# Kernel optimization log

Measured on AMD Instinct MI355X. Metric: run time of the kernel, lower is better.

Reference implementation:

```python
import jax, jax.numpy as jnp
import numpy as np

N, E, H, CIN = 10000, 320000, 4, 64
NT, ET = 8, 22
C1 = CIN          # per-head dim layer1 -> concat gives H*C1 = 256
C2 = H * CIN      # per-head dim layer2 = 256, mean over heads -> 256


def _hgat_layer(x, edge_index, node_type, edge_attr, edge_type,
                W, b, Wedge, ntemb, etemb, asrc, adst, aedge, res_proj, concat):
    Nn = x.shape[0]
    Hh, Cc = asrc.shape
    src, dst = edge_index[0], edge_index[1]
    # node-type conditioned transform: [N, H, C]
    xh = ((x + ntemb[node_type]) @ W).reshape(Nn, Hh, Cc)
    # edge features with edge-type embedding: [E, H, C]
    e = (edge_attr @ Wedge + etemb[edge_type]).reshape(-1, Hh, Cc)
    xs = xh[src]                     # [E, H, C] gather
    xd = xh[dst]                     # [E, H, C] gather
    logits = jax.nn.leaky_relu(
        (xs * asrc).sum(-1) + (xd * adst).sum(-1) + (e * aedge).sum(-1),
        negative_slope=0.2)          # [E, H]
    # segment softmax over incoming edges of each dst node
    m = jax.ops.segment_max(logits, dst, num_segments=Nn)   # [N, H]
    m = jnp.where(jnp.isfinite(m), m, jnp.zeros_like(m))
    p = jnp.exp(logits - m[dst])                            # [E, H]
    denom = jax.ops.segment_sum(p, dst, num_segments=Nn)    # [N, H]
    alpha = p / (denom[dst] + 1e-16)                        # [E, H]
    msg = alpha[..., None] * (xs + e)                       # [E, H, C]
    out = jax.ops.segment_sum(msg, dst, num_segments=Nn)    # [N, H, C]
    out = out.reshape(Nn, Hh * Cc) if concat else out.mean(axis=1)
    out = out + b
    res = x @ res_proj if res_proj is not None else x
    return out + res


def setup_inputs() -> dict:
    key = jax.random.key(0)
    ks = jax.random.split(key, 24)

    def rn(k, shape, fan_in):
        return jax.random.normal(k, shape, jnp.float32) * (fan_in ** -0.5)

    x = jax.random.normal(ks[0], (N, CIN), jnp.float32)
    edge_index = jax.random.randint(ks[1], (2, E), 0, N, jnp.int64)
    node_type = jax.random.randint(ks[2], (N,), 0, NT, jnp.int64)
    edge_attr = jax.random.normal(ks[3], (E, CIN), jnp.float32)
    edge_type = jax.random.randint(ks[4], (E,), 0, ET, jnp.int64)

    inp = dict(x=x, edge_index=edge_index, node_type=node_type,
               edge_attr=edge_attr, edge_type=edge_type)
    # layer 1: in=CIN, per-head C1, concat -> H*C1
    inp.update(
        l1_W=rn(ks[5], (CIN, H * C1), CIN),
        l1_b=rn(ks[6], (H * C1,), H * C1),
        l1_Wedge=rn(ks[7], (CIN, H * C1), CIN),
        l1_ntemb=rn(ks[8], (NT, CIN), CIN),
        l1_etemb=rn(ks[9], (ET, H * C1), H * C1),
        l1_asrc=rn(ks[10], (H, C1), C1),
        l1_adst=rn(ks[11], (H, C1), C1),
        l1_aedge=rn(ks[12], (H, C1), C1),
        l1_res=rn(ks[13], (CIN, H * C1), CIN),
    )
    # layer 2: in=H*C1, per-head C2, mean over heads -> C2
    inp.update(
        l2_W=rn(ks[14], (H * C1, H * C2), H * C1),
        l2_b=rn(ks[15], (C2,), C2),
        l2_Wedge=rn(ks[16], (CIN, H * C2), CIN),
        l2_ntemb=rn(ks[17], (NT, H * C1), H * C1),
        l2_etemb=rn(ks[18], (ET, H * C2), H * C2),
        l2_asrc=rn(ks[19], (H, C2), C2),
        l2_adst=rn(ks[20], (H, C2), C2),
        l2_aedge=rn(ks[21], (H, C2), C2),
    )
    return inp


def reference(x, edge_index, node_type, edge_attr, edge_type,
              l1_W, l1_b, l1_Wedge, l1_ntemb, l1_etemb, l1_asrc, l1_adst, l1_aedge, l1_res,
              l2_W, l2_b, l2_Wedge, l2_ntemb, l2_etemb, l2_asrc, l2_adst, l2_aedge):
    h = _hgat_layer(x, edge_index, node_type, edge_attr, edge_type,
                    l1_W, l1_b, l1_Wedge, l1_ntemb, l1_etemb,
                    l1_asrc, l1_adst, l1_aedge, l1_res, concat=True)
    h = jax.nn.relu(h)
    out = _hgat_layer(h, edge_index, node_type, edge_attr, edge_type,
                      l2_W, l2_b, l2_Wedge, l2_ntemb, l2_etemb,
                      l2_asrc, l2_adst, l2_aedge, None, concat=False)
    return out
```

## Files before the change

### kernel.cpp

```cpp
#include <hip/hip_runtime.h>
#include <stdint.h>

#define NN   10000
#define NE   320000
#define K1   704
#define K2V  1408

typedef unsigned short u16;
typedef unsigned int   u32;

__device__ __forceinline__ float b2f(u16 v){ u32 u = ((u32)v) << 16; return __uint_as_float(u); }
__device__ __forceinline__ u16 f2b(float f){
  u32 u = __float_as_uint(f);
  u32 r = (u + 0x7fffu + ((u >> 16) & 1u)) >> 16;
  return (u16)r;
}
__device__ __forceinline__ float ldf(const void* p, size_t i, int bf){
  if (bf){ u32 u = ((u32)((const u16*)p)[i]) << 16; return __uint_as_float(u); }
  return ((const float*)p)[i];
}
__device__ __forceinline__ int geti(const int* p, size_t i, int w64){
  return w64 ? p[2 * i] : p[i];
}

#define FW_W1A  0
#define FW_W1D  256
#define FW_WA12 512
#define FW_ETA1 1024
#define FW_ETA2 1112
#define FW_NTS1 1200
#define FW_NTD1 1232
#define FW_W2A  1264
#define FW_W2D  2288
#define FW_NTS2 3312
#define FW_NTD2 3344

#define WS_FLG   0u
#define WS_DEG   16u
#define WS_OFF   40016u
#define WS_CUR   80032u
#define WS_META  120032u
#define WS_EL    5240032u
#define WS_S1    15480032u
#define WS_D1    15640032u
#define WS_S2    15800032u
#define WS_D2    15960032u
#define WS_FW    16120032u
#define WS_M1T   16136032u
#define WS_M2T   16496480u
#define WS_HBUF  17217376u
#define WS_V     22337376u

__global__ void k_probe(const u16* x16, const int* ei, const int* nt, const int* et, int4* flg){
  if (threadIdx.x == 0 && blockIdx.x == 0){
    int okb = 1;
    for (int i = 0; i < 64; i++){
      u16 u = x16[i]; int e = (u >> 7) & 0xFF;
      if (!(e >= 90 && e <= 160)){ okb = 0; break; }
    }
    int ei64 = 1, nt64 = 1, et64 = 1;
    for (int i = 0; i < 32; i++){
      if (ei[2 * i + 1] != 0) ei64 = 0;
      if (nt[2 * i + 1] != 0) nt64 = 0;
      if (et[2 * i + 1] != 0) et64 = 0;
    }
    int4 f; f.x = okb; f.y = ei64; f.z = nt64; f.w = et64;
    *flg = f;
  }
}

__global__ void k_zero(int* deg){
  int t = blockIdx.x * 256 + threadIdx.x;
  if (t < NN) deg[t] = 0;
}

__global__ void k_hist(const int* ei, int* deg, const int4* flg){
  int4 f = *flg;
  int e = blockIdx.x * 256 + threadIdx.x;
  if (e < NE){ int dst = geti(ei, NE + e, f.y); atomicAdd(&deg[dst], 1); }
}

__global__ void k_scan(const int* deg, int* off, int* cursor){
  __shared__ int part[256];
  int t = threadIdx.x;
  int base = t * 40;
  int s = 0;
  for (int i = 0; i < 40; i++){ int idx = base + i; s += (idx < NN) ? deg[idx] : 0; }
  part[t] = s;
  __syncthreads();
  for (int d = 1; d < 256; d <<= 1){
    int v = (t >= d) ? part[t - d] : 0;
    __syncthreads();
    part[t] += v;
    __syncthreads();
  }
  int run = (t == 0) ? 0 : part[t - 1];
  for (int i = 0; i < 40; i++){
    int idx = base + i;
    if (idx < NN){ off[idx] = run; cursor[idx] = run; run += deg[idx]; }
  }
  if (t == 255) off[NN] = part[255];
}

__global__ void k_scatter(const int* ei, const int* ntype, const int* etype,
                          int* cursor, int4* meta, const int4* flg){
  int4 f = *flg;
  int e = blockIdx.x * 256 + threadIdx.x;
  if (e < NE){
    int src = geti(ei, e, f.y), dst = geti(ei, NE + e, f.y);
    int pos = atomicAdd(&cursor[dst], 1);
    int4 m; m.x = e; m.y = src; m.z = geti(etype, e, f.w); m.w = geti(ntype, src, f.z);
    meta[pos] = m;
  }
}

__global__ void k_fold_a(const void* W1, const void* Wedge1, const void* asrc1, const void* adst1,
                         const void* aedge1, const void* etemb1,
                         const void* W2, const void* Wedge2, const void* asrc2, const void* adst2,
                         const void* aedge2, const void* etemb2, float* fw, const int4* flg){
  int bf = flg->x;
  int s = blockIdx.x * 256 + threadIdx.x;
  if (s < 256){
    int k = s >> 2, h = s & 3; float a = 0.f, d = 0.f;
    for (int c = 0; c < 64; c++){
      float w = ldf(W1, k * 256 + h * 64 + c, bf);
      a += w * ldf(asrc1, h * 64 + c, bf); d += w * ldf(adst1, h * 64 + c, bf);
    }
    fw[FW_W1A + k * 4 + h] = a; fw[FW_W1D + k * 4 + h] = d;
  } else if (s < 768){
    int q = s - 256; int k = q >> 3, dd = q & 7; float a = 0.f;
    if (dd < 4){
      for (int c = 0; c < 64; c++) a += ldf(Wedge1, k * 256 + dd * 64 + c, bf) * ldf(aedge1, dd * 64 + c, bf);
    } else {
      int h = dd - 4;
      for (int c = 0; c < 256; c++) a += ldf(Wedge2, k * 1024 + h * 256 + c, bf) * ldf(aedge2, h * 256 + c, bf);
    }
    fw[FW_WA12 + k * 8 + dd] = a;
  } else if (s < 856){
    int q = s - 768; int te = q >> 2, h = q & 3; float a = 0.f;
    for (int c = 0; c < 64; c++) a += ldf(etemb1, te * 256 + h * 64 + c, bf) * ldf(aedge1, h * 64 + c, bf);
    fw[FW_ETA1 + te * 4 + h] = a;
  } else if (s < 944){
    int q = s - 856; int te = q >> 2, h = q & 3; float a = 0.f;
    for (int c = 0; c < 256; c++) a += ldf(etemb2, te * 1024 + h * 256 + c, bf) * ldf(aedge2, h * 256 + c, bf);
    fw[FW_ETA2 + te * 4 + h] = a;
  } else if (s < 1968){
    int q = s - 944; int k = q >> 2, h = q & 3; float a = 0.f, d = 0.f;
    for (int c = 0; c < 256; c++){
      float w = ldf(W2, k * 1024 + h * 256 + c, bf);
      a += w * ldf(asrc2, h * 256 + c, bf); d += w * ldf(adst2, h * 256 + c, bf);
    }
    fw[FW_W2A + k * 4 + h] = a; fw[FW_W2D + k * 4 + h] = d;
  }
}

__global__ void k_fold_b(const void* ntemb1, const void* ntemb2, float* fw, const int4* flg){
  int bf = flg->x;
  int t = threadIdx.x;
  if (t < 32){
    int te = t >> 2, h = t & 3; float a = 0.f, d = 0.f;
    for (int k = 0; k < 64; k++){
      float x = ldf(ntemb1, te * 64 + k, bf);
      a += x * fw[FW_W1A + k * 4 + h]; d += x * fw[FW_W1D + k * 4 + h];
    }
    fw[FW_NTS1 + te * 4 + h] = a; fw[FW_NTD1 + te * 4 + h] = d;
  } else {
    int q = t - 32; int te = q >> 2, h = q & 3; float a = 0.f, d = 0.f;
    for (int k = 0; k < 256; k++){
      float x = ldf(ntemb2, te * 256 + k, bf);
      a += x * fw[FW_W2A + k * 4 + h]; d += x * fw[FW_W2D + k * 4 + h];
    }
    fw[FW_NTS2 + te * 4 + h] = a; fw[FW_NTD2 + te * 4 + h] = d;
  }
}

__global__ void k_m1t(const void* W1, const void* Wedge1, const void* ntemb1, const void* etemb1,
                      const void* res1, const void* b1, u16* M1T, const int4* flg){
  int bf = flg->x;
  int c = blockIdx.x; int t = threadIdx.x; int ch = c >> 6;
  for (int r = t; r < K1; r += 256){
    float v = 0.f;
    if (r < 256){ int h = r >> 6, k = r & 63; v = (h == ch) ? ldf(W1, k * 256 + c, bf) : 0.f; }
    else if (r < 512){ int q = r - 256; int h = q >> 6, k = q & 63; v = (h == ch) ? ldf(Wedge1, k * 256 + c, bf) : 0.f; }
    else if (r < 544){ int q = r - 512; int h = q >> 3, te = q & 7;
      if (h == ch){ float a = 0.f; for (int k = 0; k < 64; k++) a += ldf(ntemb1, te * 64 + k, bf) * ldf(W1, k * 256 + c, bf); v = a; } }
    else if (r < 632){ int q = r - 544; int h = q / 22, te = q % 22; v = (h == ch) ? ldf(etemb1, te * 256 + c, bf) : 0.f; }
    else if (r < 696){ int k = r - 632; v = ldf(res1, k * 256 + c, bf); }
    else if (r == 696){ v = ldf(b1, c, bf); }
    M1T[c * K1 + r] = f2b(v);
  }
}

__global__ void k_m2t(const void* W2, const void* Wedge2, const void* ntemb2, const void* etemb2,
                      const void* b2, u16* M2T, const int4* flg){
  int bf = flg->x;
  int c = blockIdx.x; int t = threadIdx.x;
  for (int r = t; r < K2V; r += 256){
    float v = 0.f;
    if (r < 1024){ int h = r >> 8, k = r & 255; v = 0.25f * ldf(W2, k * 1024 + h * 256 + c, bf); }
    else if (r < 1280){ int q = r - 1024; int h = q >> 6, k = q & 63; v = 0.25f * ldf(Wedge2, k * 1024 + h * 256 + c, bf); }
    else if (r < 1312){ int q = r - 1280; int h = q >> 3, te = q & 7; float a = 0.f;
      for (int k = 0; k < 256; k++) a += ldf(ntemb2, te * 256 + k, bf) * ldf(W2, k * 1024 + h * 256 + c, bf);
      v = 0.25f * a; }
    else if (r < 1400){ int q = r - 1312; int h = q / 22, te = q % 22; v = 0.25f * ldf(etemb2, te * 1024 + h * 256 + c, bf); }
    else if (r == 1400){ v = ldf(b2, c, bf); }
    M2T[c * K2V + r] = f2b(v);
  }
}

__global__ void k_sd1(const void* x, const int* ntype, const float* fw, float* s1, float* d1,
                      const int4* flg){
  int4 f = *flg;
  int id = blockIdx.x * 256 + threadIdx.x;
  if (id >= NN * 4) return;
  int n = id >> 2, h = id & 3;
  float a = 0.f, d = 0.f;
  for (int k = 0; k < 64; k++){
    float xv = ldf(x, (size_t)n * 64 + k, f.x);
    a += xv * fw[FW_W1A + k * 4 + h]; d += xv * fw[FW_W1D + k * 4 + h];
  }
  int nt = geti(ntype, n, f.z);
  s1[id] = a + fw[FW_NTS1 + nt * 4 + h];
  d1[id] = d + fw[FW_NTD1 + nt * 4 + h];
}

__global__ void k_sd2(const u16* hbuf, const int* ntype, const float* fw, float* s2, float* d2,
                      const int4* flg){
  int4 f = *flg;
  int id = blockIdx.x * 256 + threadIdx.x;
  if (id >= NN * 4) return;
  int n = id >> 2, h = id & 3;
  float a = 0.f, d = 0.f;
  for (int k = 0; k < 256; k++){
    float xv = b2f(hbuf[n * 256 + k]);
    a += xv * fw[FW_W2A + k * 4 + h]; d += xv * fw[FW_W2D + k * 4 + h];
  }
  int nt = geti(ntype, n, f.z);
  s2[id] = a + fw[FW_NTS2 + nt * 4 + h];
  d2[id] = d + fw[FW_NTD2 + nt * 4 + h];
}

__global__ void k_el(const void* ea, const int* etype, const float* fw, float* el, const int4* flg){
  __shared__ float sw[512];
  __shared__ float sea[32 * 65];
  int4 f = *flg;
  int t = threadIdx.x;
  for (int i = t; i < 512; i += 256) sw[i] = fw[FW_WA12 + i];
  int e0 = blockIdx.x * 32;
  {
    int eloc = t >> 3, kc = (t & 7) * 8;
    float* dp = &sea[eloc * 65 + kc];
    if (f.x){
      const u16* p = (const u16*)ea + (size_t)(e0 + eloc) * 64 + kc;
      ushort4 a = *(const ushort4*)p;
      ushort4 b = *(const ushort4*)(p + 4);
      dp[0] = b2f(a.x); dp[1] = b2f(a.y); dp[2] = b2f(a.z); dp[3] = b2f(a.w);
      dp[4] = b2f(b.x); dp[5] = b2f(b.y); dp[6] = b2f(b.z); dp[7] = b2f(b.w);
    } else {
      const float* p = (const float*)ea + (size_t)(e0 + eloc) * 64 + kc;
      float4 a = *(const float4*)p;
      float4 b = *(const float4*)(p + 4);
      dp[0] = a.x; dp[1] = a.y; dp[2] = a.z; dp[3] = a.w;
      dp[4] = b.x; dp[5] = b.y; dp[6] = b.z; dp[7] = b.w;
    }
  }
  __syncthreads();
  int eloc = t >> 3, d = t & 7;
  int e = e0 + eloc;
  float a = 0.f;
  for (int k = 0; k < 64; k++) a += sea[eloc * 65 + k] * sw[k * 8 + d];
  int et = geti(etype, e, f.w);
  a += (d < 4) ? fw[FW_ETA1 + et * 4 + d] : fw[FW_ETA2 + et * 4 + (d - 4)];
  el[(size_t)e * 8 + d] = a;
}

__global__ __launch_bounds__(256) void k_agg1(const int* off, const int4* meta,
    const float* el, const float* s1, const float* d1,
    const void* x, const void* ea, u16* V1, const int4* flg){
  int bf = flg->x;
  int n = blockIdx.x * 4 + (threadIdx.x >> 6);
  int lane = threadIdx.x & 63;
  int beg = off[n], end = off[n + 1];
  float4 dv = *(const float4*)&d1[n * 4];
  float dvh[4] = {dv.x, dv.y, dv.z, dv.w};

  int ht1 = lane >> 3;
  int c1  = lane & 7;
  int ht2a = lane / 22;
  int c2a  = lane - 22 * ht2a;
  bool v2b = (lane >= 2 && lane < 24);
  int c2b  = lane - 2;

  float den[4] = {0.f, 0.f, 0.f, 0.f};
  float g1[4] = {0.f, 0.f, 0.f, 0.f};
  float g2[4] = {0.f, 0.f, 0.f, 0.f};
  float t1 = 0.f, t2a = 0.f, t2b = 0.f;
#pragma unroll 2
  for (int i = beg; i < end; i++){
    int4 md = meta[i];
    int eid = md.x, src = md.y, et = md.z, nt = md.w;
    float4 elv = *(const float4*)&el[(size_t)eid * 8];
    float4 sv  = *(const float4*)&s1[src * 4];
    float lg[4] = {sv.x + dvh[0] + elv.x, sv.y + dvh[1] + elv.y,
                   sv.z + dvh[2] + elv.z, sv.w + dvh[3] + elv.w};
    float pa[4];
#pragma unroll
    for (int h = 0; h < 4; h++){
      float l = lg[h]; l = fmaxf(l, 0.2f * l);
      float p = __expf(l);
      den[h] += p; pa[h] = p;
    }
    float xv = ldf(x, (size_t)src * 64 + lane, bf);
    float ev = ldf(ea, (size_t)eid * 64 + lane, bf);
#pragma unroll
    for (int h = 0; h < 4; h++){ g1[h] += pa[h] * xv; g2[h] += pa[h] * ev; }
    float pt1 = (ht1 & 2) ? ((ht1 & 1) ? pa[3] : pa[2]) : ((ht1 & 1) ? pa[1] : pa[0]);
    t1  += ((ht1 < 4) && (nt == c1)) ? pt1 : 0.f;
    float p2a = (ht2a == 2) ? pa[2] : ((ht2a == 1) ? pa[1] : pa[0]);
    t2a += (et == c2a) ? p2a : 0.f;
    t2b += (v2b && (et == c2b)) ? pa[3] : 0.f;
  }
  float inv[4];
#pragma unroll
  for (int h = 0; h < 4; h++)
    inv[h] = (den[h] > 0.f) ? 1.f / (den[h] + 1e-16f) : 0.f;

  u16* vrow = &V1[(size_t)n * K1];
#pragma unroll
  for (int h = 0; h < 4; h++){
    vrow[h * 64 + lane]       = f2b(inv[h] * g1[h]);
    vrow[256 + h * 64 + lane] = f2b(inv[h] * g2[h]);
  }
  if (lane < 32) vrow[512 + lane] = f2b(inv[lane >> 3] * t1);
  vrow[544 + lane] = f2b(inv[ht2a] * t2a);
  if (lane < 24) vrow[608 + lane] = f2b(inv[3] * t2b * ((lane >= 2) ? 1.f : 0.f) + ((lane < 2) ? inv[2] * t2b : 0.f));
  vrow[632 + lane] = f2b(ldf(x, (size_t)n * 64 + lane, bf));
  if (lane == 0) vrow[696] = f2b(1.f);
  if (lane >= 1 && lane < 8) vrow[696 + lane] = 0;
}

__global__ __launch_bounds__(256) void k_agg2(const int* off, const int4* meta,
    const float* el, const float* s2, const float* d2,
    const u16* hbuf, const void* ea, u16* V2, int nbase, const int4* flg){
  int bf = flg->x;
  int nl = blockIdx.x * 4 + (threadIdx.x >> 6);
  int n = nbase + nl;
  int lane = threadIdx.x & 63;
  int beg = off[n], end = off[n + 1];
  float4 dv = *(const float4*)&d2[n * 4];
  float dvh[4] = {dv.x, dv.y, dv.z, dv.w};

  int ht1 = lane >> 3;
  int c1  = lane & 7;
  int ht2a = lane / 22;
  int c2a  = lane - 22 * ht2a;
  bool v2b = (lane >= 2 && lane < 24);
  int c2b  = lane - 2;

  float den[4] = {0.f, 0.f, 0.f, 0.f};
  float g3[4][4] = {};
  float g4[4] = {0.f, 0.f, 0.f, 0.f};
  float t3 = 0.f, t4a = 0.f, t4b = 0.f;
#pragma unroll 2
  for (int i = beg; i < end; i++){
    int4 md = meta[i];
    int eid = md.x, src = md.y, et = md.z, nt = md.w;
    float4 elv = *(const float4*)&el[(size_t)eid * 8 + 4];
    float4 sv  = *(const float4*)&s2[src * 4];
    float lg[4] = {sv.x + dvh[0] + elv.x, sv.y + dvh[1] + elv.y,
                   sv.z + dvh[2] + elv.z, sv.w + dvh[3] + elv.w};
    float pa[4];
#pragma unroll
    for (int h = 0; h < 4; h++){
      float l = lg[h]; l = fmaxf(l, 0.2f * l);
      float p = __expf(l);
      den[h] += p; pa[h] = p;
    }
    ushort4 hv = *(const ushort4*)&hbuf[(size_t)src * 256 + lane * 4];
    float h0 = b2f(hv.x), h1 = b2f(hv.y), h2 = b2f(hv.z), h3 = b2f(hv.w);
    float ev = ldf(ea, (size_t)eid * 64 + lane, bf);
#pragma unroll
    for (int h = 0; h < 4; h++){
      float p = pa[h];
      g3[h][0] += p * h0; g3[h][1] += p * h1; g3[h][2] += p * h2; g3[h][3] += p * h3;
      g4[h] += p * ev;
    }
    float pt1 = (ht1 & 2) ? ((ht1 & 1) ? pa[3] : pa[2]) : ((ht1 & 1) ? pa[1] : pa[0]);
    t3  += ((ht1 < 4) && (nt == c1)) ? pt1 : 0.f;
    float p2a = (ht2a == 2) ? pa[2] : ((ht2a == 1) ? pa[1] : pa[0]);
    t4a += (et == c2a) ? p2a : 0.f;
    t4b += (v2b && (et == c2b)) ? pa[3] : 0.f;
  }
  float inv[4];
#pragma unroll
  for (int h = 0; h < 4; h++)
    inv[h] = (den[h] > 0.f) ? 1.f / (den[h] + 1e-16f) : 0.f;

  u16* vrow = &V2[(size_t)nl * K2V];
#pragma unroll
  for (int h = 0; h < 4; h++){
#pragma unroll
    for (int j = 0; j < 4; j++)
      vrow[h * 256 + lane * 4 + j] = f2b(inv[h] * g3[h][j]);
    vrow[1024 + h * 64 + lane] = f2b(inv[h] * g4[h]);
  }
  if (lane < 32) vrow[1280 + lane] = f2b(inv[lane >> 3] * t3);
  vrow[1312 + lane] = f2b(inv[ht2a] * t4a);
  if (lane < 24) vrow[1376 + lane] = f2b(inv[3] * t4b * ((lane >= 2) ? 1.f : 0.f) + ((lane < 2) ? inv[2] * t4b : 0.f));
  if (lane == 0) vrow[1400] = f2b(1.f);
  if (lane >= 1 && lane < 8) vrow[1400 + lane] = 0;
}

typedef __bf16 bf16x8 __attribute__((ext_vector_type(8)));
typedef float  f32x4  __attribute__((ext_vector_type(4)));

template<int KK, int MODE>
__global__ __launch_bounds__(256) void k_gemm(const u16* A, const u16* Bt,
                                              const u16* hres, void* outv,
                                              int rowbase, int mcount){
  __shared__ __align__(16) u16 As[64 * 40];
  __shared__ __align__(16) u16 Bs[64 * 40];
  int t = threadIdx.x;
  int w = t >> 6, lane = t & 63;
  int m0 = blockIdx.x * 64, n0 = blockIdx.y * 64;
  int wm = w & 1, wn = w >> 1;
  f32x4 acc[2][2] = {};
  int ar = t >> 2, akc = (t & 3) * 8;
  for (int k0 = 0; k0 < KK; k0 += 32){
    {
      int row = m0 + ar;
      ushort4 v0 = {0, 0, 0, 0}, v1 = {0, 0, 0, 0};
      if (row < mcount){
        const u16* p = &A[(size_t)row * KK + k0 + akc];
        v0 = *(const ushort4*)p; v1 = *(const ushort4*)(p + 4);
      }
      *(ushort4*)&As[ar * 40 + akc] = v0;
      *(ushort4*)&As[ar * 40 + akc + 4] = v1;
      const u16* q = &Bt[(size_t)(n0 + ar) * KK + k0 + akc];
      ushort4 b0 = *(const ushort4*)q;
      ushort4 b1 = *(const ushort4*)(q + 4);
      *(ushort4*)&Bs[ar * 40 + akc] = b0;
      *(ushort4*)&Bs[ar * 40 + akc + 4] = b1;
    }
    __syncthreads();
    int kq = (lane >> 4) * 8;
    int ml = lane & 15;
    bf16x8 a0 = *(const bf16x8*)&As[(wm * 32 + ml) * 40 + kq];
    bf16x8 a1 = *(const bf16x8*)&As[(wm * 32 + 16 + ml) * 40 + kq];
    bf16x8 b0 = *(const bf16x8*)&Bs[(wn * 32 + ml) * 40 + kq];
    bf16x8 b1 = *(const bf16x8*)&Bs[(wn * 32 + 16 + ml) * 40 + kq];
    acc[0][0] = __builtin_amdgcn_mfma_f32_16x16x32_bf16(a0, b0, acc[0][0], 0, 0, 0);
    acc[0][1] = __builtin_amdgcn_mfma_f32_16x16x32_bf16(a0, b1, acc[0][1], 0, 0, 0);
    acc[1][0] = __builtin_amdgcn_mfma_f32_16x16x32_bf16(a1, b0, acc[1][0], 0, 0, 0);
    acc[1][1] = __builtin_amdgcn_mfma_f32_16x16x32_bf16(a1, b1, acc[1][1], 0, 0, 0);
    __syncthreads();
  }
  int quad = lane >> 4, col4 = lane & 15;
#pragma unroll
  for (int i = 0; i < 2; i++)
#pragma unroll
    for (int j = 0; j < 2; j++){
      int colG = n0 + wn * 32 + j * 16 + col4;
#pragma unroll
      for (int r = 0; r < 4; r++){
        int rowL = m0 + wm * 32 + i * 16 + quad * 4 + r;
        if (rowL < mcount){
          int rowG = rowbase + rowL;
          float v = acc[i][j][r];
          if (MODE == 1){
            v = fmaxf(v, 0.f);
            ((u16*)outv)[(size_t)rowG * 256 + colG] = f2b(v);
          } else {
            v += b2f(hres[(size_t)rowG * 256 + colG]);
            ((float*)outv)[(size_t)rowG * 256 + colG] = v;
          }
        }
      }
    }
}

extern "C" void kernel_launch(void* const* d_in, const int* in_sizes, int n_in,
                              void* d_out, int out_size, void* d_ws, size_t ws_size,
                              hipStream_t stream){
  const void* x      = d_in[0];
  const int*  ei     = (const int*)d_in[1];
  const int*  ntype  = (const int*)d_in[2];
  const void* ea     = d_in[3];
  const int*  etype  = (const int*)d_in[4];
  const void* l1_W     = d_in[5];
  const void* l1_b     = d_in[6];
  const void* l1_Wedge = d_in[7];
  const void* l1_ntemb = d_in[8];
  const void* l1_etemb = d_in[9];
  const void* l1_asrc  = d_in[10];
  const void* l1_adst  = d_in[11];
  const void* l1_aedge = d_in[12];
  const void* l1_res   = d_in[13];
  const void* l2_W     = d_in[14];
  const void* l2_b     = d_in[15];
  const void* l2_Wedge = d_in[16];
  const void* l2_ntemb = d_in[17];
  const void* l2_etemb = d_in[18];
  const void* l2_asrc  = d_in[19];
  const void* l2_adst  = d_in[20];
  const void* l2_aedge = d_in[21];

  char* ws = (char*)d_ws;
  int4*  flg    = (int4*)(ws + WS_FLG);
  int*   deg    = (int*)(ws + WS_DEG);
  int*   off    = (int*)(ws + WS_OFF);
  int*   cur    = (int*)(ws + WS_CUR);
  int4*  meta   = (int4*)(ws + WS_META);
  float* el     = (float*)(ws + WS_EL);
  float* s1     = (float*)(ws + WS_S1);
  float* d1     = (float*)(ws + WS_D1);
  float* s2     = (float*)(ws + WS_S2);
  float* d2     = (float*)(ws + WS_D2);
  float* fw     = (float*)(ws + WS_FW);
  u16*   M1T    = (u16*)(ws + WS_M1T);
  u16*   M2T    = (u16*)(ws + WS_M2T);
  u16*   hbuf   = (u16*)(ws + WS_HBUF);
  u16*   V      = (u16*)(ws + WS_V);

  hipLaunchKernelGGL(k_probe,   dim3(1),    dim3(64),  0, stream,
                     (const u16*)x, ei, ntype, etype, flg);
  hipLaunchKernelGGL(k_zero,    dim3(40),   dim3(256), 0, stream, deg);
  hipLaunchKernelGGL(k_hist,    dim3(1250), dim3(256), 0, stream, ei, deg, flg);
  hipLaunchKernelGGL(k_scan,    dim3(1),    dim3(256), 0, stream, deg, off, cur);
  hipLaunchKernelGGL(k_scatter, dim3(1250), dim3(256), 0, stream, ei, ntype, etype, cur, meta, flg);
  hipLaunchKernelGGL(k_fold_a,  dim3(8),    dim3(256), 0, stream,
                     l1_W, l1_Wedge, l1_asrc, l1_adst, l1_aedge, l1_etemb,
                     l2_W, l2_Wedge, l2_asrc, l2_adst, l2_aedge, l2_etemb, fw, flg);
  hipLaunchKernelGGL(k_fold_b,  dim3(1),    dim3(64),  0, stream, l1_ntemb, l2_ntemb, fw, flg);
  hipLaunchKernelGGL(k_m1t,     dim3(256),  dim3(256), 0, stream,
                     l1_W, l1_Wedge, l1_ntemb, l1_etemb, l1_res, l1_b, M1T, flg);
  hipLaunchKernelGGL(k_m2t,     dim3(256),  dim3(256), 0, stream,
                     l2_W, l2_Wedge, l2_ntemb, l2_etemb, l2_b, M2T, flg);
  hipLaunchKernelGGL(k_sd1,     dim3(157),  dim3(256), 0, stream, x, ntype, fw, s1, d1, flg);
  hipLaunchKernelGGL(k_el,      dim3(10000),dim3(256), 0, stream, ea, etype, fw, el, flg);
  hipLaunchKernelGGL(k_agg1,    dim3(2500), dim3(256), 0, stream, off, meta, el, s1, d1, x, ea, V, flg);
  hipLaunchKernelGGL((k_gemm<K1, 1>),  dim3(157, 4), dim3(256), 0, stream, V, M1T, hbuf, (void*)hbuf, 0, NN);
  hipLaunchKernelGGL(k_sd2,     dim3(157),  dim3(256), 0, stream, hbuf, ntype, fw, s2, d2, flg);
  for (int c = 0; c < 2; c++){
    int base = c * 5000;
    hipLaunchKernelGGL(k_agg2,  dim3(1250), dim3(256), 0, stream,
                       off, meta, el, s2, d2, hbuf, ea, V, base, flg);
    hipLaunchKernelGGL((k_gemm<K2V, 2>), dim3(79, 4), dim3(256), 0, stream,
                       V, M2T, hbuf, d_out, base, 5000);
  }
}
```

Baseline: 606.0 us.

## Precompute per-edge attention exponentials in edge order and cache bf16 edge features

```diff
diff --git a/kernel.cpp b/kernel.cpp
--- a/kernel.cpp
+++ b/kernel.cpp
@@ -40,7 +40,8 @@
 #define WS_OFF   40016u
 #define WS_CUR   80032u
 #define WS_META  120032u
-#define WS_EL    5240032u
+#define WS_P1    5240032u
+#define WS_EL2   10360032u
 #define WS_S1    15480032u
 #define WS_D1    15640032u
 #define WS_S2    15800032u
@@ -50,6 +51,8 @@
 #define WS_M2T   16496480u
 #define WS_HBUF  17217376u
 #define WS_V     22337376u
+#define WS_EA16  36417376u
+#define WS_NEED16 77377376ull
 
 __global__ void k_probe(const u16* x16, const int* ei, const int* nt, const int* et, int4* flg){
   if (threadIdx.x == 0 && blockIdx.x == 0){
@@ -240,7 +243,9 @@
   d2[id] = d + fw[FW_NTD2 + nt * 4 + h];
 }
 
-__global__ void k_el(const void* ea, const int* etype, const float* fw, float* el, const int4* flg){
+__global__ void k_el(const void* ea, const int* etype, const int* ei,
+                     const float* s1, const float* d1, const float* fw,
+                     float* p1, float* el2, u16* ea16, const int4* flg){
   __shared__ float sw[512];
   __shared__ float sea[32 * 65];
   int4 f = *flg;
@@ -249,19 +254,30 @@
   int e0 = blockIdx.x * 32;
   {
     int eloc = t >> 3, kc = (t & 7) * 8;
-    float* dp = &sea[eloc * 65 + kc];
+    int e = e0 + eloc;
+    float v[8];
     if (f.x){
-      const u16* p = (const u16*)ea + (size_t)(e0 + eloc) * 64 + kc;
+      const u16* p = (const u16*)ea + (size_t)e * 64 + kc;
       ushort4 a = *(const ushort4*)p;
       ushort4 b = *(const ushort4*)(p + 4);
-      dp[0] = b2f(a.x); dp[1] = b2f(a.y); dp[2] = b2f(a.z); dp[3] = b2f(a.w);
-      dp[4] = b2f(b.x); dp[5] = b2f(b.y); dp[6] = b2f(b.z); dp[7] = b2f(b.w);
+      v[0] = b2f(a.x); v[1] = b2f(a.y); v[2] = b2f(a.z); v[3] = b2f(a.w);
+      v[4] = b2f(b.x); v[5] = b2f(b.y); v[6] = b2f(b.z); v[7] = b2f(b.w);
     } else {
-      const float* p = (const float*)ea + (size_t)(e0 + eloc) * 64 + kc;
+      const float* p = (const float*)ea + (size_t)e * 64 + kc;
       float4 a = *(const float4*)p;
       float4 b = *(const float4*)(p + 4);
-      dp[0] = a.x; dp[1] = a.y; dp[2] = a.z; dp[3] = a.w;
-      dp[4] = b.x; dp[5] = b.y; dp[6] = b.z; dp[7] = b.w;
+      v[0] = a.x; v[1] = a.y; v[2] = a.z; v[3] = a.w;
+      v[4] = b.x; v[5] = b.y; v[6] = b.z; v[7] = b.w;
+    }
+    float* dp = &sea[eloc * 65 + kc];
+#pragma unroll
+    for (int j = 0; j < 8; j++) dp[j] = v[j];
+    if (ea16){
+      ushort4 o0, o1;
+      o0.x = f2b(v[0]); o0.y = f2b(v[1]); o0.z = f2b(v[2]); o0.w = f2b(v[3]);
+      o1.x = f2b(v[4]); o1.y = f2b(v[5]); o1.z = f2b(v[6]); o1.w = f2b(v[7]);
+      *(ushort4*)&ea16[(size_t)e * 64 + kc]     = o0;
+      *(ushort4*)&ea16[(size_t)e * 64 + kc + 4] = o1;
     }
   }
   __syncthreads();
@@ -270,26 +286,45 @@
   float a = 0.f;
   for (int k = 0; k < 64; k++) a += sea[eloc * 65 + k] * sw[k * 8 + d];
   int et = geti(etype, e, f.w);
-  a += (d < 4) ? fw[FW_ETA1 + et * 4 + d] : fw[FW_ETA2 + et * 4 + (d - 4)];
-  el[(size_t)e * 8 + d] = a;
+  if (d < 4){
+    a += fw[FW_ETA1 + et * 4 + d];
+    int src = geti(ei, e, f.y), dst = geti(ei, NE + e, f.y);
+    float l = s1[src * 4 + d] + d1[dst * 4 + d] + a;
+    l = fmaxf(l, 0.2f * l);
+    p1[(size_t)e * 4 + d] = __expf(l);
+  } else {
+    a += fw[FW_ETA2 + et * 4 + (d - 4)];
+    el2[(size_t)e * 4 + (d - 4)] = a;
+  }
+}
+
+__global__ void k_p2(const int* ei, const float* el2, const float* s2, const float* d2,
+                     float* p2, const int4* flg){
+  int4 f = *flg;
+  int idx = blockIdx.x * 256 + threadIdx.x;
+  if (idx >= NE * 4) return;
+  int e = idx >> 2, h = idx & 3;
+  int src = geti(ei, e, f.y), dst = geti(ei, NE + e, f.y);
+  float l = s2[src * 4 + h] + d2[dst * 4 + h] + el2[idx];
+  l = fmaxf(l, 0.2f * l);
+  p2[idx] = __expf(l);
 }
 
 __global__ __launch_bounds__(256) void k_agg1(const int* off, const int4* meta,
-    const float* el, const float* s1, const float* d1,
-    const void* x, const void* ea, u16* V1, const int4* flg){
+    const float* p1, const void* x, const void* ea, const u16* ea16,
+    u16* V1, const int4* flg){
   int bf = flg->x;
   int n = blockIdx.x * 4 + (threadIdx.x >> 6);
   int lane = threadIdx.x & 63;
   int beg = off[n], end = off[n + 1];
-  float4 dv = *(const float4*)&d1[n * 4];
-  float dvh[4] = {dv.x, dv.y, dv.z, dv.w};
 
   int ht1 = lane >> 3;
   int c1  = lane & 7;
   int ht2a = lane / 22;
   int c2a  = lane - 22 * ht2a;
-  bool v2b = (lane >= 2 && lane < 24);
-  int c2b  = lane - 2;
+  int hb   = (lane < 2) ? 2 : 3;
+  int cb   = (lane < 2) ? (20 + lane) : (lane - 2);
+  bool vb  = (lane < 24);
 
   float den[4] = {0.f, 0.f, 0.f, 0.f};
   float g1[4] = {0.f, 0.f, 0.f, 0.f};
@@ -299,26 +334,19 @@
   for (int i = beg; i < end; i++){
     int4 md = meta[i];
     int eid = md.x, src = md.y, et = md.z, nt = md.w;
-    float4 elv = *(const float4*)&el[(size_t)eid * 8];
-    float4 sv  = *(const float4*)&s1[src * 4];
-    float lg[4] = {sv.x + dvh[0] + elv.x, sv.y + dvh[1] + elv.y,
-                   sv.z + dvh[2] + elv.z, sv.w + dvh[3] + elv.w};
-    float pa[4];
-#pragma unroll
-    for (int h = 0; h < 4; h++){
-      float l = lg[h]; l = fmaxf(l, 0.2f * l);
-      float p = __expf(l);
-      den[h] += p; pa[h] = p;
-    }
+    float4 p4 = *(const float4*)&p1[(size_t)eid * 4];
+    float pa[4] = {p4.x, p4.y, p4.z, p4.w};
+    den[0] += pa[0]; den[1] += pa[1]; den[2] += pa[2]; den[3] += pa[3];
     float xv = ldf(x, (size_t)src * 64 + lane, bf);
-    float ev = ldf(ea, (size_t)eid * 64 + lane, bf);
+    float ev = ea16 ? b2f(ea16[(size_t)eid * 64 + lane]) : ldf(ea, (size_t)eid * 64 + lane, bf);
 #pragma unroll
     for (int h = 0; h < 4; h++){ g1[h] += pa[h] * xv; g2[h] += pa[h] * ev; }
     float pt1 = (ht1 & 2) ? ((ht1 & 1) ? pa[3] : pa[2]) : ((ht1 & 1) ? pa[1] : pa[0]);
     t1  += ((ht1 < 4) && (nt == c1)) ? pt1 : 0.f;
     float p2a = (ht2a == 2) ? pa[2] : ((ht2a == 1) ? pa[1] : pa[0]);
     t2a += (et == c2a) ? p2a : 0.f;
-    t2b += (v2b && (et == c2b)) ? pa[3] : 0.f;
+    float pb = (lane < 2) ? pa[2] : pa[3];
+    t2b += (vb && (et == cb)) ? pb : 0.f;
   }
   float inv[4];
 #pragma unroll
@@ -333,29 +361,28 @@
   }
   if (lane < 32) vrow[512 + lane] = f2b(inv[lane >> 3] * t1);
   vrow[544 + lane] = f2b(inv[ht2a] * t2a);
-  if (lane < 24) vrow[608 + lane] = f2b(inv[3] * t2b * ((lane >= 2) ? 1.f : 0.f) + ((lane < 2) ? inv[2] * t2b : 0.f));
+  if (lane < 24) vrow[608 + lane] = f2b(inv[hb] * t2b);
   vrow[632 + lane] = f2b(ldf(x, (size_t)n * 64 + lane, bf));
   if (lane == 0) vrow[696] = f2b(1.f);
   if (lane >= 1 && lane < 8) vrow[696 + lane] = 0;
 }
 
 __global__ __launch_bounds__(256) void k_agg2(const int* off, const int4* meta,
-    const float* el, const float* s2, const float* d2,
-    const u16* hbuf, const void* ea, u16* V2, int nbase, const int4* flg){
+    const float* p2, const u16* hbuf, const void* ea, const u16* ea16,
+    u16* V2, int nbase, const int4* flg){
   int bf = flg->x;
   int nl = blockIdx.x * 4 + (threadIdx.x >> 6);
   int n = nbase + nl;
   int lane = threadIdx.x & 63;
   int beg = off[n], end = off[n + 1];
-  float4 dv = *(const float4*)&d2[n * 4];
-  float dvh[4] = {dv.x, dv.y, dv.z, dv.w};
 
   int ht1 = lane >> 3;
   int c1  = lane & 7;
   int ht2a = lane / 22;
   int c2a  = lane - 22 * ht2a;
-  bool v2b = (lane >= 2 && lane < 24);
-  int c2b  = lane - 2;
+  int hb   = (lane < 2) ? 2 : 3;
+  int cb   = (lane < 2) ? (20 + lane) : (lane - 2);
+  bool vb  = (lane < 24);
 
   float den[4] = {0.f, 0.f, 0.f, 0.f};
   float g3[4][4] = {};
@@ -365,20 +392,12 @@
   for (int i = beg; i < end; i++){
     int4 md = meta[i];
     int eid = md.x, src = md.y, et = md.z, nt = md.w;
-    float4 elv = *(const float4*)&el[(size_t)eid * 8 + 4];
-    float4 sv  = *(const float4*)&s2[src * 4];
-    float lg[4] = {sv.x + dvh[0] + elv.x, sv.y + dvh[1] + elv.y,
-                   sv.z + dvh[2] + elv.z, sv.w + dvh[3] + elv.w};
-    float pa[4];
-#pragma unroll
-    for (int h = 0; h < 4; h++){
-      float l = lg[h]; l = fmaxf(l, 0.2f * l);
-      float p = __expf(l);
-      den[h] += p; pa[h] = p;
-    }
+    float4 p4 = *(const float4*)&p2[(size_t)eid * 4];
+    float pa[4] = {p4.x, p4.y, p4.z, p4.w};
+    den[0] += pa[0]; den[1] += pa[1]; den[2] += pa[2]; den[3] += pa[3];
     ushort4 hv = *(const ushort4*)&hbuf[(size_t)src * 256 + lane * 4];
     float h0 = b2f(hv.x), h1 = b2f(hv.y), h2 = b2f(hv.z), h3 = b2f(hv.w);
-    float ev = ldf(ea, (size_t)eid * 64 + lane, bf);
+    float ev = ea16 ? b2f(ea16[(size_t)eid * 64 + lane]) : ldf(ea, (size_t)eid * 64 + lane, bf);
 #pragma unroll
     for (int h = 0; h < 4; h++){
       float p = pa[h];
@@ -389,7 +408,8 @@
     t3  += ((ht1 < 4) && (nt == c1)) ? pt1 : 0.f;
     float p2a = (ht2a == 2) ? pa[2] : ((ht2a == 1) ? pa[1] : pa[0]);
     t4a += (et == c2a) ? p2a : 0.f;
-    t4b += (v2b && (et == c2b)) ? pa[3] : 0.f;
+    float pb = (lane < 2) ? pa[2] : pa[3];
+    t4b += (vb && (et == cb)) ? pb : 0.f;
   }
   float inv[4];
 #pragma unroll
@@ -406,7 +426,7 @@
   }
   if (lane < 32) vrow[1280 + lane] = f2b(inv[lane >> 3] * t3);
   vrow[1312 + lane] = f2b(inv[ht2a] * t4a);
-  if (lane < 24) vrow[1376 + lane] = f2b(inv[3] * t4b * ((lane >= 2) ? 1.f : 0.f) + ((lane < 2) ? inv[2] * t4b : 0.f));
+  if (lane < 24) vrow[1376 + lane] = f2b(inv[hb] * t4b);
   if (lane == 0) vrow[1400] = f2b(1.f);
   if (lane >= 1 && lane < 8) vrow[1400 + lane] = 0;
 }
@@ -511,7 +531,9 @@
   int*   off    = (int*)(ws + WS_OFF);
   int*   cur    = (int*)(ws + WS_CUR);
   int4*  meta   = (int4*)(ws + WS_META);
-  float* el     = (float*)(ws + WS_EL);
+  float* p1     = (float*)(ws + WS_P1);
+  float* el2    = (float*)(ws + WS_EL2);
+  float* p2     = (float*)(ws + WS_P1);
   float* s1     = (float*)(ws + WS_S1);
   float* d1     = (float*)(ws + WS_D1);
   float* s2     = (float*)(ws + WS_S2);
@@ -521,6 +543,7 @@
   u16*   M2T    = (u16*)(ws + WS_M2T);
   u16*   hbuf   = (u16*)(ws + WS_HBUF);
   u16*   V      = (u16*)(ws + WS_V);
+  u16*   ea16   = (ws_size >= WS_NEED16) ? (u16*)(ws + WS_EA16) : (u16*)0;
 
   hipLaunchKernelGGL(k_probe,   dim3(1),    dim3(64),  0, stream,
                      (const u16*)x, ei, ntype, etype, flg);
@@ -537,14 +560,17 @@
   hipLaunchKernelGGL(k_m2t,     dim3(256),  dim3(256), 0, stream,
                      l2_W, l2_Wedge, l2_ntemb, l2_etemb, l2_b, M2T, flg);
   hipLaunchKernelGGL(k_sd1,     dim3(157),  dim3(256), 0, stream, x, ntype, fw, s1, d1, flg);
-  hipLaunchKernelGGL(k_el,      dim3(10000),dim3(256), 0, stream, ea, etype, fw, el, flg);
-  hipLaunchKernelGGL(k_agg1,    dim3(2500), dim3(256), 0, stream, off, meta, el, s1, d1, x, ea, V, flg);
+  hipLaunchKernelGGL(k_el,      dim3(10000),dim3(256), 0, stream,
+                     ea, etype, ei, s1, d1, fw, p1, el2, ea16, flg);
+  hipLaunchKernelGGL(k_agg1,    dim3(2500), dim3(256), 0, stream,
+                     off, meta, p1, x, ea, ea16, V, flg);
   hipLaunchKernelGGL((k_gemm<K1, 1>),  dim3(157, 4), dim3(256), 0, stream, V, M1T, hbuf, (void*)hbuf, 0, NN);
   hipLaunchKernelGGL(k_sd2,     dim3(157),  dim3(256), 0, stream, hbuf, ntype, fw, s2, d2, flg);
+  hipLaunchKernelGGL(k_p2,      dim3(5000), dim3(256), 0, stream, ei, el2, s2, d2, p2, flg);
   for (int c = 0; c < 2; c++){
     int base = c * 5000;
     hipLaunchKernelGGL(k_agg2,  dim3(1250), dim3(256), 0, stream,
-                       off, meta, el, s2, d2, hbuf, ea, V, base, flg);
+                       off, meta, p2, hbuf, ea, ea16, V, base, flg);
     hipLaunchKernelGGL((k_gemm<K2V, 2>), dim3(79, 4), dim3(256), 0, stream,
                        V, M2T, hbuf, d_out, base, 5000);
   }
```

New measurement: 610.7 us. About the same (+0.8%).
